# Kernel optimization log

Hardware: AMD Instinct MI355X
Metric: run time of the kernel (lower is better)

Reference implementation:

```python
import jax, jax.numpy as jnp
import numpy as np

N = 50000      # nodes
E = 600000     # edges
D = 128        # hidden_dim (bottleneck=1)
G = 64         # graphs in batch
GN_EPS = 1e-5  # GraphNorm eps


def setup_inputs() -> dict:
    key = jax.random.key(0)
    ks = jax.random.split(key, 10)
    node_h = jax.random.normal(ks[0], (N, D), dtype=jnp.float32)
    edge_attr = jax.random.normal(ks[1], (E, D), dtype=jnp.float32)
    batch = jnp.sort(jax.random.randint(ks[2], (N,), 0, G)).astype(jnp.int64)
    edge_index = jax.random.randint(ks[3], (2, E), 0, N).astype(jnp.int64)
    # params: lin1, conv.lin (edge linear), conv.eps, GraphNorm(weight,bias,mean_scale)
    w1 = jax.random.normal(ks[4], (D, D), dtype=jnp.float32) * 0.02
    b1 = jnp.zeros((D,), dtype=jnp.float32)
    we = jax.random.normal(ks[5], (D, D), dtype=jnp.float32) * 0.02
    be = jnp.zeros((D,), dtype=jnp.float32)
    eps = jnp.zeros((), dtype=jnp.float32)  # train_eps, init 0
    gn_weight = jnp.ones((D,), dtype=jnp.float32)
    gn_bias = jnp.zeros((D,), dtype=jnp.float32)
    gn_mean_scale = jnp.ones((D,), dtype=jnp.float32)
    return {"node_h": node_h, "edge_attr": edge_attr, "batch": batch,
            "edge_index": edge_index, "w1": w1, "b1": b1, "we": we, "be": be,
            "eps": eps, "gn_weight": gn_weight, "gn_bias": gn_bias,
            "gn_mean_scale": gn_mean_scale}


def graph_norm(x, batch, weight, bias, mean_scale):
    ones = jnp.ones((x.shape[0],), dtype=x.dtype)
    cnt = jnp.maximum(jax.ops.segment_sum(ones, batch, num_segments=G), 1.0)[:, None]
    mean = jax.ops.segment_sum(x, batch, num_segments=G) / cnt
    out = x - mean[batch] * mean_scale
    var = jax.ops.segment_sum(out * out, batch, num_segments=G) / cnt
    std = jnp.sqrt(var + GN_EPS)
    return weight * out / std[batch] + bias


def reference(node_h, edge_attr, batch, edge_index, w1, b1, we, be, eps,
              gn_weight, gn_bias, gn_mean_scale):
    h = node_h @ w1.T + b1                                  # lin1: [N, D]
    src, dst = edge_index[0], edge_index[1]
    # GINEConvMod message: SiLU(x_j + lin(edge_attr)); gather -> add -> act
    msg = jax.nn.silu(h[src] + (edge_attr @ we.T + be))     # [E, D]
    agg = jax.ops.segment_sum(msg, dst, num_segments=N)     # scatter-add
    conv = (1.0 + eps) * h + agg                            # nn = Identity
    # dropout(p=0) and lin2=Identity are no-ops
    out = jax.nn.silu(conv)
    return graph_norm(out + node_h, batch, gn_weight, gn_bias, gn_mean_scale)
```

## Files before the change

### kernel.cpp

```cpp
#include <hip/hip_runtime.h>
#include <hip/hip_bf16.h>

#define NN 50000
#define NE 600000
#define DIM 128
#define NG 64

using bf16x8 = __attribute__((ext_vector_type(8))) __bf16;
using f32x4  = __attribute__((ext_vector_type(4))) float;

__device__ __forceinline__ bf16x8 cvt8(const float* __restrict__ p) {
    f32x4 a = *(const f32x4*)p;
    f32x4 b = *(const f32x4*)(p + 4);
    bf16x8 r;
    #pragma unroll
    for (int i = 0; i < 4; ++i) { r[i] = (__bf16)a[i]; r[i + 4] = (__bf16)b[i]; }
    return r;
}

__device__ __forceinline__ void stage_weights(const float* __restrict__ W, __bf16* sW) {
    for (int i = threadIdx.x; i < 128 * 16; i += 256) {
        int row = i >> 4, seg = i & 15;
        *(bf16x8*)(&sW[row * 136 + seg * 8]) = cvt8(W + row * 128 + seg * 8);
    }
    __syncthreads();
}

__global__ __launch_bounds__(256) void gemm_bias(
    const float* __restrict__ X, const float* __restrict__ W,
    const float* __restrict__ bias, float* __restrict__ Y, int M)
{
    __shared__ __bf16 sW[128 * 136];
    stage_weights(W, sW);

    int wave = threadIdx.x >> 6, lane = threadIdx.x & 63;
    int col = lane & 15, quad = lane >> 4;
    int tile = (blockIdx.x * 4 + wave) * 16;
    if (tile >= M) return;

    f32x4 acc[8] = {};
    const float* xp = X + (size_t)(tile + col) * DIM + quad * 8;
    #pragma unroll
    for (int k0 = 0; k0 < 128; k0 += 32) {
        bf16x8 a = cvt8(xp + k0);
        #pragma unroll
        for (int t = 0; t < 8; ++t) {
            bf16x8 b = *(const bf16x8*)(&sW[(t * 16 + col) * 136 + k0 + quad * 8]);
            acc[t] = __builtin_amdgcn_mfma_f32_16x16x32_bf16(a, b, acc[t], 0, 0, 0);
        }
    }

    float bv[8];
    #pragma unroll
    for (int t = 0; t < 8; ++t) bv[t] = bias[t * 16 + col];
    #pragma unroll
    for (int r = 0; r < 4; ++r) {
        float* yp = Y + (size_t)(tile + quad * 4 + r) * DIM;
        #pragma unroll
        for (int t = 0; t < 8; ++t) yp[t * 16 + col] = acc[t][r] + bv[t];
    }
}

__global__ __launch_bounds__(256) void edge_msg(
    const float* __restrict__ EA, const float* __restrict__ W,
    const float* __restrict__ bias,
    const int* __restrict__ src, const int* __restrict__ dst,
    const float* __restrict__ H, float* __restrict__ AGG)
{
    __shared__ __bf16 sW[128 * 136];
    stage_weights(W, sW);

    int wave = threadIdx.x >> 6, lane = threadIdx.x & 63;
    int col = lane & 15, quad = lane >> 4;
    int tile = (blockIdx.x * 4 + wave) * 16;

    f32x4 acc[8] = {};
    const float* xp = EA + (size_t)(tile + col) * DIM + quad * 8;
    #pragma unroll
    for (int k0 = 0; k0 < 128; k0 += 32) {
        bf16x8 a = cvt8(xp + k0);
        #pragma unroll
        for (int t = 0; t < 8; ++t) {
            bf16x8 b = *(const bf16x8*)(&sW[(t * 16 + col) * 136 + k0 + quad * 8]);
            acc[t] = __builtin_amdgcn_mfma_f32_16x16x32_bf16(a, b, acc[t], 0, 0, 0);
        }
    }

    float bv[8];
    #pragma unroll
    for (int t = 0; t < 8; ++t) bv[t] = bias[t * 16 + col];

    #pragma unroll
    for (int r = 0; r < 4; ++r) {
        int e = tile + quad * 4 + r;
        int s  = src[e];
        int dd = dst[e];
        const float* hp = H + (size_t)s * DIM;
        float* ap = AGG + (size_t)dd * DIM;
        #pragma unroll
        for (int t = 0; t < 8; ++t) {
            int d = t * 16 + col;
            float v = acc[t][r] + bv[t] + hp[d];
            v = v / (1.f + __expf(-v));
            atomicAdd(&ap[d], v);
        }
    }
}

__global__ __launch_bounds__(128) void fuse_x_stats(
    float* __restrict__ H, const float* __restrict__ AGG,
    const float* __restrict__ node_h, const float* __restrict__ epsp,
    const int* __restrict__ batch,
    float* __restrict__ SUMS, float* __restrict__ CNT, int M)
{
    int d = threadIdx.x;
    int n0 = blockIdx.x * 64;
    int nend = min(n0 + 64, M);
    float epsv = 1.f + epsp[0];

    int cur_g = batch[n0];
    float run = 0.f; int runlen = 0;
    for (int n = n0; n < nend; ++n) {
        int g = batch[n];
        if (g != cur_g) {
            atomicAdd(&SUMS[cur_g * DIM + d], run);
            if (d == 0) atomicAdd(&CNT[cur_g], (float)runlen);
            run = 0.f; runlen = 0; cur_g = g;
        }
        size_t idx = (size_t)n * DIM + d;
        float v = epsv * H[idx] + AGG[idx];
        v = v / (1.f + __expf(-v));
        v += node_h[idx];
        H[idx] = v;
        run += v; runlen++;
    }
    atomicAdd(&SUMS[cur_g * DIM + d], run);
    if (d == 0) atomicAdd(&CNT[cur_g], (float)runlen);
}

__global__ __launch_bounds__(128) void var_pass(
    const float* __restrict__ X, const int* __restrict__ batch,
    const float* __restrict__ msc,
    const float* __restrict__ SUMS, const float* __restrict__ CNT,
    float* __restrict__ VARS, int M)
{
    int d = threadIdx.x;
    int n0 = blockIdx.x * 64;
    int nend = min(n0 + 64, M);
    float ms = msc[d];

    int cur_g = batch[n0];
    float c = fmaxf(CNT[cur_g], 1.f);
    float mean = SUMS[cur_g * DIM + d] / c;
    float run = 0.f;
    for (int n = n0; n < nend; ++n) {
        int g = batch[n];
        if (g != cur_g) {
            atomicAdd(&VARS[cur_g * DIM + d], run);
            run = 0.f; cur_g = g;
            c = fmaxf(CNT[g], 1.f);
            mean = SUMS[g * DIM + d] / c;
        }
        float v = X[(size_t)n * DIM + d] - mean * ms;
        run += v * v;
    }
    atomicAdd(&VARS[cur_g * DIM + d], run);
}

__global__ __launch_bounds__(128) void finalize(
    const float* __restrict__ X, const int* __restrict__ batch,
    const float* __restrict__ msc,
    const float* __restrict__ SUMS, const float* __restrict__ VARS,
    const float* __restrict__ CNT,
    const float* __restrict__ gw, const float* __restrict__ gb,
    float* __restrict__ OUT, int M)
{
    int d = threadIdx.x;
    int n0 = blockIdx.x * 64;
    int nend = min(n0 + 64, M);
    float ms = msc[d];
    float wd = gw[d];
    float bd = gb[d];

    int cur_g = -1;
    float mean = 0.f, rstd = 0.f;
    for (int n = n0; n < nend; ++n) {
        int g = batch[n];
        if (g != cur_g) {
            cur_g = g;
            float c = fmaxf(CNT[g], 1.f);
            mean = SUMS[g * DIM + d] / c;
            rstd = rsqrtf(VARS[g * DIM + d] / c + 1e-5f);
        }
        size_t idx = (size_t)n * DIM + d;
        float v = X[idx] - mean * ms;
        OUT[idx] = wd * v * rstd + bd;
    }
}

extern "C" void kernel_launch(void* const* d_in, const int* in_sizes, int n_in,
                              void* d_out, int out_size, void* d_ws, size_t ws_size,
                              hipStream_t stream) {
    const float* node_h    = (const float*)d_in[0];
    const float* edge_attr = (const float*)d_in[1];
    const int*   batch     = (const int*)d_in[2];
    const int*   eidx      = (const int*)d_in[3];
    const float* w1        = (const float*)d_in[4];
    const float* b1        = (const float*)d_in[5];
    const float* we        = (const float*)d_in[6];
    const float* be        = (const float*)d_in[7];
    const float* eps       = (const float*)d_in[8];
    const float* gnw       = (const float*)d_in[9];
    const float* gnb       = (const float*)d_in[10];
    const float* gnms      = (const float*)d_in[11];

    float* ws   = (float*)d_ws;
    float* H    = ws;
    float* AGG  = ws + 6400000;
    float* SUMS = ws + 12800000;
    float* VARS = SUMS + NG * DIM;
    float* CNT  = VARS + NG * DIM;

    hipMemsetAsync(AGG, 0, (size_t)(6400000 + NG * DIM * 2 + NG) * sizeof(float), stream);

    gemm_bias<<<782, 256, 0, stream>>>(node_h, w1, b1, H, NN);
    edge_msg<<<9375, 256, 0, stream>>>(edge_attr, we, be, eidx, eidx + NE, H, AGG);
    fuse_x_stats<<<782, 128, 0, stream>>>(H, AGG, node_h, eps, batch, SUMS, CNT, NN);
    var_pass<<<782, 128, 0, stream>>>(H, batch, gnms, SUMS, CNT, VARS, NN);
    finalize<<<782, 128, 0, stream>>>(H, batch, gnms, SUMS, VARS, CNT, gnw, gnb,
                                      (float*)d_out, NN);
}
```

Baseline: 762.3 us.

## Replace atomic scatter-add with CSR counting-sort and bf16 message gather

```diff
diff --git a/kernel.cpp b/kernel.cpp
--- a/kernel.cpp
+++ b/kernel.cpp
@@ -5,6 +5,7 @@
 #define NE 600000
 #define DIM 128
 #define NG 64
+#define NCHUNK 98
 
 using bf16x8 = __attribute__((ext_vector_type(8))) __bf16;
 using f32x4  = __attribute__((ext_vector_type(4))) float;
@@ -49,7 +50,6 @@
             acc[t] = __builtin_amdgcn_mfma_f32_16x16x32_bf16(a, b, acc[t], 0, 0, 0);
         }
     }
-
     float bv[8];
     #pragma unroll
     for (int t = 0; t < 8; ++t) bv[t] = bias[t * 16 + col];
@@ -61,11 +61,73 @@
     }
 }
 
-__global__ __launch_bounds__(256) void edge_msg(
+__global__ __launch_bounds__(256) void k_hist(const int* __restrict__ dst, int* __restrict__ deg) {
+    int e = blockIdx.x * 256 + threadIdx.x;
+    if (e < NE) atomicAdd(&deg[dst[e]], 1);
+}
+
+__global__ __launch_bounds__(256) void k_scan_a(const int* __restrict__ deg, int* __restrict__ chunkSum) {
+    __shared__ int s[256];
+    int c = blockIdx.x, t = threadIdx.x;
+    int b = c * 512 + t;
+    int v = (b < NN) ? deg[b] : 0;
+    if (b + 256 < NN) v += deg[b + 256];
+    s[t] = v; __syncthreads();
+    for (int off = 128; off > 0; off >>= 1) {
+        if (t < off) s[t] += s[t + off];
+        __syncthreads();
+    }
+    if (t == 0) chunkSum[c] = s[0];
+}
+
+__global__ __launch_bounds__(128) void k_scan_b(const int* __restrict__ chunkSum,
+                                                int* __restrict__ chunkOff, int* __restrict__ rowptr) {
+    __shared__ int s[128];
+    int t = threadIdx.x;
+    int v = (t < NCHUNK) ? chunkSum[t] : 0;
+    s[t] = v; __syncthreads();
+    for (int off = 1; off < 128; off <<= 1) {
+        int x = (t >= off) ? s[t - off] : 0;
+        __syncthreads();
+        s[t] += x;
+        __syncthreads();
+    }
+    chunkOff[t] = s[t] - v;
+    if (t == 0) rowptr[NN] = NE;
+}
+
+__global__ __launch_bounds__(512) void k_scan_c(const int* __restrict__ deg,
+                                                const int* __restrict__ chunkOff,
+                                                int* __restrict__ rowptr, int* __restrict__ pos) {
+    __shared__ int s[512];
+    int c = blockIdx.x, t = threadIdx.x;
+    int i = c * 512 + t;
+    int v = (i < NN) ? deg[i] : 0;
+    s[t] = v; __syncthreads();
+    for (int off = 1; off < 512; off <<= 1) {
+        int x = (t >= off) ? s[t - off] : 0;
+        __syncthreads();
+        s[t] += x;
+        __syncthreads();
+    }
+    if (i < NN) { rowptr[i] = chunkOff[c] + s[t] - v; pos[i] = 0; }
+}
+
+__global__ __launch_bounds__(256) void k_slot(const int* __restrict__ dst,
+                                              const int* __restrict__ rowptr,
+                                              int* __restrict__ pos, int* __restrict__ slot) {
+    int e = blockIdx.x * 256 + threadIdx.x;
+    if (e >= NE) return;
+    int d = dst[e];
+    int p = atomicAdd(&pos[d], 1);
+    slot[e] = rowptr[d] + p;
+}
+
+__global__ __launch_bounds__(256) void edge_msg_sorted(
     const float* __restrict__ EA, const float* __restrict__ W,
     const float* __restrict__ bias,
-    const int* __restrict__ src, const int* __restrict__ dst,
-    const float* __restrict__ H, float* __restrict__ AGG)
+    const int* __restrict__ src, const int* __restrict__ slot,
+    const float* __restrict__ H, __hip_bfloat16* __restrict__ MSG)
 {
     __shared__ __bf16 sW[128 * 136];
     stage_weights(W, sW);
@@ -85,7 +147,6 @@
             acc[t] = __builtin_amdgcn_mfma_f32_16x16x32_bf16(a, b, acc[t], 0, 0, 0);
         }
     }
-
     float bv[8];
     #pragma unroll
     for (int t = 0; t < 8; ++t) bv[t] = bias[t * 16 + col];
@@ -94,30 +155,43 @@
     for (int r = 0; r < 4; ++r) {
         int e = tile + quad * 4 + r;
         int s  = src[e];
-        int dd = dst[e];
+        int sl = slot[e];
         const float* hp = H + (size_t)s * DIM;
-        float* ap = AGG + (size_t)dd * DIM;
+        __hip_bfloat16* mp = MSG + (size_t)sl * DIM;
         #pragma unroll
         for (int t = 0; t < 8; ++t) {
             int d = t * 16 + col;
             float v = acc[t][r] + bv[t] + hp[d];
             v = v / (1.f + __expf(-v));
-            atomicAdd(&ap[d], v);
-        }
-    }
-}
-
-__global__ __launch_bounds__(128) void fuse_x_stats(
-    float* __restrict__ H, const float* __restrict__ AGG,
-    const float* __restrict__ node_h, const float* __restrict__ epsp,
-    const int* __restrict__ batch,
-    float* __restrict__ SUMS, float* __restrict__ CNT, int M)
+            mp[d] = __float2bfloat16(v);
+        }
+    }
+}
+
+__global__ __launch_bounds__(128) void k_gather(
+    const __hip_bfloat16* __restrict__ MSG, const int* __restrict__ rowptr,
+    float* __restrict__ H, const float* __restrict__ node_h,
+    const float* __restrict__ epsp)
+{
+    int n = blockIdx.x, d = threadIdx.x;
+    int s = rowptr[n], epos = rowptr[n + 1];
+    float acc = 0.f;
+    for (int e = s; e < epos; ++e)
+        acc += __bfloat162float(MSG[(size_t)e * DIM + d]);
+    size_t idx = (size_t)n * DIM + d;
+    float v = (1.f + epsp[0]) * H[idx] + acc;
+    v = v / (1.f + __expf(-v));
+    H[idx] = v + node_h[idx];
+}
+
+__global__ __launch_bounds__(128) void stats_pass(
+    const float* __restrict__ X, const int* __restrict__ batch,
+    float* __restrict__ SUMS, float* __restrict__ CNT, int npb)
 {
     int d = threadIdx.x;
-    int n0 = blockIdx.x * 64;
-    int nend = min(n0 + 64, M);
-    float epsv = 1.f + epsp[0];
-
+    int n0 = blockIdx.x * npb;
+    int nend = min(n0 + npb, NN);
+    if (n0 >= NN) return;
     int cur_g = batch[n0];
     float run = 0.f; int runlen = 0;
     for (int n = n0; n < nend; ++n) {
@@ -127,12 +201,7 @@
             if (d == 0) atomicAdd(&CNT[cur_g], (float)runlen);
             run = 0.f; runlen = 0; cur_g = g;
         }
-        size_t idx = (size_t)n * DIM + d;
-        float v = epsv * H[idx] + AGG[idx];
-        v = v / (1.f + __expf(-v));
-        v += node_h[idx];
-        H[idx] = v;
-        run += v; runlen++;
+        run += X[(size_t)n * DIM + d]; runlen++;
     }
     atomicAdd(&SUMS[cur_g * DIM + d], run);
     if (d == 0) atomicAdd(&CNT[cur_g], (float)runlen);
@@ -142,13 +211,13 @@
     const float* __restrict__ X, const int* __restrict__ batch,
     const float* __restrict__ msc,
     const float* __restrict__ SUMS, const float* __restrict__ CNT,
-    float* __restrict__ VARS, int M)
+    float* __restrict__ VARS, int npb)
 {
     int d = threadIdx.x;
-    int n0 = blockIdx.x * 64;
-    int nend = min(n0 + 64, M);
+    int n0 = blockIdx.x * npb;
+    int nend = min(n0 + npb, NN);
+    if (n0 >= NN) return;
     float ms = msc[d];
-
     int cur_g = batch[n0];
     float c = fmaxf(CNT[cur_g], 1.f);
     float mean = SUMS[cur_g * DIM + d] / c;
@@ -173,15 +242,13 @@
     const float* __restrict__ SUMS, const float* __restrict__ VARS,
     const float* __restrict__ CNT,
     const float* __restrict__ gw, const float* __restrict__ gb,
-    float* __restrict__ OUT, int M)
+    float* __restrict__ OUT, int npb)
 {
     int d = threadIdx.x;
-    int n0 = blockIdx.x * 64;
-    int nend = min(n0 + 64, M);
-    float ms = msc[d];
-    float wd = gw[d];
-    float bd = gb[d];
-
+    int n0 = blockIdx.x * npb;
+    int nend = min(n0 + npb, NN);
+    if (n0 >= NN) return;
+    float ms = msc[d], wd = gw[d], bd = gb[d];
     int cur_g = -1;
     float mean = 0.f, rstd = 0.f;
     for (int n = n0; n < nend; ++n) {
@@ -195,6 +262,64 @@
         size_t idx = (size_t)n * DIM + d;
         float v = X[idx] - mean * ms;
         OUT[idx] = wd * v * rstd + bd;
+    }
+}
+
+__global__ __launch_bounds__(256) void edge_msg_atomic(
+    const float* __restrict__ EA, const float* __restrict__ W,
+    const float* __restrict__ bias,
+    const int* __restrict__ src, const int* __restrict__ dst,
+    const float* __restrict__ H, float* __restrict__ AGG)
+{
+    __shared__ __bf16 sW[128 * 136];
+    stage_weights(W, sW);
+    int wave = threadIdx.x >> 6, lane = threadIdx.x & 63;
+    int col = lane & 15, quad = lane >> 4;
+    int tile = (blockIdx.x * 4 + wave) * 16;
+    f32x4 acc[8] = {};
+    const float* xp = EA + (size_t)(tile + col) * DIM + quad * 8;
+    #pragma unroll
+    for (int k0 = 0; k0 < 128; k0 += 32) {
+        bf16x8 a = cvt8(xp + k0);
+        #pragma unroll
+        for (int t = 0; t < 8; ++t) {
+            bf16x8 b = *(const bf16x8*)(&sW[(t * 16 + col) * 136 + k0 + quad * 8]);
+            acc[t] = __builtin_amdgcn_mfma_f32_16x16x32_bf16(a, b, acc[t], 0, 0, 0);
+        }
+    }
+    float bv[8];
+    #pragma unroll
+    for (int t = 0; t < 8; ++t) bv[t] = bias[t * 16 + col];
+    #pragma unroll
+    for (int r = 0; r < 4; ++r) {
+        int e = tile + quad * 4 + r;
+        int s = src[e], dd = dst[e];
+        const float* hp = H + (size_t)s * DIM;
+        float* ap = AGG + (size_t)dd * DIM;
+        #pragma unroll
+        for (int t = 0; t < 8; ++t) {
+            int d = t * 16 + col;
+            float v = acc[t][r] + bv[t] + hp[d];
+            v = v / (1.f + __expf(-v));
+            atomicAdd(&ap[d], v);
+        }
+    }
+}
+
+__global__ __launch_bounds__(128) void fuse_x_atomic(
+    float* __restrict__ H, const float* __restrict__ AGG,
+    const float* __restrict__ node_h, const float* __restrict__ epsp, int npb)
+{
+    int d = threadIdx.x;
+    int n0 = blockIdx.x * npb;
+    int nend = min(n0 + npb, NN);
+    if (n0 >= NN) return;
+    float epsv = 1.f + epsp[0];
+    for (int n = n0; n < nend; ++n) {
+        size_t idx = (size_t)n * DIM + d;
+        float v = epsv * H[idx] + AGG[idx];
+        v = v / (1.f + __expf(-v));
+        H[idx] = v + node_h[idx];
     }
 }
 
@@ -213,20 +338,61 @@
     const float* gnw       = (const float*)d_in[9];
     const float* gnb       = (const float*)d_in[10];
     const float* gnms      = (const float*)d_in[11];
-
-    float* ws   = (float*)d_ws;
-    float* H    = ws;
-    float* AGG  = ws + 6400000;
-    float* SUMS = ws + 12800000;
-    float* VARS = SUMS + NG * DIM;
-    float* CNT  = VARS + NG * DIM;
-
-    hipMemsetAsync(AGG, 0, (size_t)(6400000 + NG * DIM * 2 + NG) * sizeof(float), stream);
-
-    gemm_bias<<<782, 256, 0, stream>>>(node_h, w1, b1, H, NN);
-    edge_msg<<<9375, 256, 0, stream>>>(edge_attr, we, be, eidx, eidx + NE, H, AGG);
-    fuse_x_stats<<<782, 128, 0, stream>>>(H, AGG, node_h, eps, batch, SUMS, CNT, NN);
-    var_pass<<<782, 128, 0, stream>>>(H, batch, gnms, SUMS, CNT, VARS, NN);
-    finalize<<<782, 128, 0, stream>>>(H, batch, gnms, SUMS, VARS, CNT, gnw, gnb,
-                                      (float*)d_out, NN);
-}
+    const int* src = eidx, * dst = eidx + NE;
+
+    char* base = (char*)d_ws;
+    float* H = (float*)base;
+
+    size_t oMSG   = 25600000;
+    size_t oROW   = oMSG + 153600000;
+    size_t oDEG   = oROW + 200064;
+    size_t oSUMS  = oDEG + 200000;
+    size_t oVARS  = oSUMS + 32768;
+    size_t oCNT   = oVARS + 32768;
+    size_t oSLOT  = oCNT + 256;
+    size_t oCSA   = oSLOT + 2400000;
+    size_t oCSB   = oCSA + 512;
+    size_t needed = oCSB + 512;
+
+    bool fast = ws_size >= needed;
+
+    if (fast) {
+        __hip_bfloat16* MSG = (__hip_bfloat16*)(base + oMSG);
+        int* rowptr = (int*)(base + oROW);
+        int* deg    = (int*)(base + oDEG);
+        float* SUMS = (float*)(base + oSUMS);
+        float* VARS = (float*)(base + oVARS);
+        float* CNT  = (float*)(base + oCNT);
+        int* slot   = (int*)(base + oSLOT);
+        int* csum   = (int*)(base + oCSA);
+        int* coff   = (int*)(base + oCSB);
+
+        hipMemsetAsync(deg, 0, 200000 + 32768 + 32768 + 256, stream);
+
+        gemm_bias<<<782, 256, 0, stream>>>(node_h, w1, b1, H, NN);
+        k_hist  <<<(NE + 255) / 256, 256, 0, stream>>>(dst, deg);
+        k_scan_a<<<NCHUNK, 256, 0, stream>>>(deg, csum);
+        k_scan_b<<<1, 128, 0, stream>>>(csum, coff, rowptr);
+        k_scan_c<<<NCHUNK, 512, 0, stream>>>(deg, coff, rowptr, deg );
+        k_slot  <<<(NE + 255) / 256, 256, 0, stream>>>(dst, rowptr, deg, slot);
+        edge_msg_sorted<<<9375, 256, 0, stream>>>(edge_attr, we, be, src, slot, H, MSG);
+        k_gather<<<NN, 128, 0, stream>>>(MSG, rowptr, H, node_h, eps);
+        stats_pass<<<3125, 128, 0, stream>>>(H, batch, SUMS, CNT, 16);
+        var_pass  <<<3125, 128, 0, stream>>>(H, batch, gnms, SUMS, CNT, VARS, 16);
+        finalize  <<<3125, 128, 0, stream>>>(H, batch, gnms, SUMS, VARS, CNT, gnw, gnb,
+                                             (float*)d_out, 16);
+    } else {
+        float* AGG  = H + 6400000;
+        float* SUMS = H + 12800000;
+        float* VARS = SUMS + NG * DIM;
+        float* CNT  = VARS + NG * DIM;
+        hipMemsetAsync(AGG, 0, (size_t)(6400000 + NG * DIM * 2 + NG) * sizeof(float), stream);
+        gemm_bias<<<782, 256, 0, stream>>>(node_h, w1, b1, H, NN);
+        edge_msg_atomic<<<9375, 256, 0, stream>>>(edge_attr, we, be, src, dst, H, AGG);
+        fuse_x_atomic<<<3125, 128, 0, stream>>>(H, AGG, node_h, eps, 16);
+        stats_pass<<<3125, 128, 0, stream>>>(H, batch, SUMS, CNT, 16);
+        var_pass  <<<3125, 128, 0, stream>>>(H, batch, gnms, SUMS, CNT, VARS, 16);
+        finalize  <<<3125, 128, 0, stream>>>(H, batch, gnms, SUMS, VARS, CNT, gnw, gnb,
+                                             (float*)d_out, 16);
+    }
+}
```

Measured after the change: 724.7 us. 1.05x faster.
